# Kernel optimization log

Measured on AMD Instinct MI355X. Metric: run time of the kernel, lower is better.

The kernel has to match this reference:

```python
import jax, jax.numpy as jnp
import numpy as np
import math

EPS = 1e-5
ANGLES = [0, 30, 45, 60, 90, 135]
SIGMA = 0.3
POOL = 7  # top-hat neighbourhood


def make_masks(H, W):
    # Soft Gaussian stripe masks, one per angle: [A, H, W]
    ys = np.linspace(-1.0, 1.0, H)
    xs = np.linspace(-1.0, 1.0, W)
    gy, gx = np.meshgrid(ys, xs, indexing='ij')
    ms = []
    for a in ANGLES:
        t = a * math.pi / 180.0
        perp = gx * (-math.sin(t)) + gy * math.cos(t)
        ms.append(np.exp(-0.5 * (perp / SIGMA) ** 2))
    return jnp.asarray(np.stack(ms, axis=0), dtype=jnp.float32)


def dwconv1d(x, w):
    # x: [B, C, L], w: [C, 1, K] depthwise, 'same' padding (odd K)
    return jax.lax.conv_general_dilated(
        x, w, window_strides=(1,), padding='SAME',
        feature_group_count=x.shape[1],
        dimension_numbers=('NCH', 'OIH', 'NCH'))


def bn(x, gamma, beta, axes, pshape):
    # Training-mode batch norm (biased variance, as in torch forward)
    mean = x.mean(axes, keepdims=True)
    var = x.var(axes, keepdims=True)
    return (x - mean) * jax.lax.rsqrt(var + EPS) * gamma.reshape(pshape) + beta.reshape(pshape)


def maxpool_same(x, k):
    # torch MaxPool2d(k, stride=1, padding=k//2): pad with -inf
    p = k // 2
    return jax.lax.reduce_window(
        x, -jnp.inf, jax.lax.max,
        window_dimensions=(1, 1, k, k), window_strides=(1, 1, 1, 1),
        padding=[(0, 0), (0, 0), (p, p), (p, p)])


def setup_inputs() -> dict:
    key = jax.random.key(0)
    ks = jax.random.split(key, 8)
    B, C, H, W = 128, 576, 28, 28
    K = 3
    x = jax.random.normal(ks[0], (B, C, H, W), dtype=jnp.float32)
    h_w = jax.random.normal(ks[1], (C, 1, K), dtype=jnp.float32) * 0.2
    v_w = jax.random.normal(ks[2], (C, 1, K), dtype=jnp.float32) * 0.2
    f_w = jax.random.normal(ks[3], (C,), dtype=jnp.float32) * 0.2  # 1x1 dw conv = per-channel scale
    h_g = jnp.ones((C,), jnp.float32); h_b = jnp.zeros((C,), jnp.float32)
    v_g = jnp.ones((C,), jnp.float32); v_b = jnp.zeros((C,), jnp.float32)
    f_g = jnp.ones((C,), jnp.float32); f_b = jnp.zeros((C,), jnp.float32)
    return {"x": x, "h_w": h_w, "h_g": h_g, "h_b": h_b,
            "v_w": v_w, "v_g": v_g, "v_b": v_b,
            "f_w": f_w, "f_g": f_g, "f_b": f_b}


def reference(x, h_w, h_g, h_b, v_w, v_g, v_b, f_w, f_g, f_b):
    B, C, H, W = x.shape
    # Horizontal stream: mean over W -> dw conv1d over H -> BN1d -> sigmoid -> [B,C,H,1]
    ph = x.mean(axis=-1)                                   # [B, C, H]
    A_h = jax.nn.sigmoid(bn(dwconv1d(ph, h_w), h_g, h_b, (0, 2), (1, C, 1)))[..., None]
    # Vertical stream: mean over H -> dw conv1d over W -> BN1d -> sigmoid -> [B,C,1,W]
    pv = x.mean(axis=-2)                                   # [B, C, W]
    A_v = jax.nn.sigmoid(bn(dwconv1d(pv, v_w), v_g, v_b, (0, 2), (1, C, 1)))[:, :, None, :]
    # Focal spot stream: white top-hat -> per-channel scale -> BN2d -> sigmoid
    spots = maxpool_same(x, POOL) - x                      # [B, C, H, W]
    A_f = jax.nn.sigmoid(bn(spots * f_w[None, :, None, None], f_g, f_b, (0, 2, 3), (1, C, 1, 1)))
    # Orientation bank: masked global means, sigmoid per angle, mean over angles
    masks = make_masks(H, W)                               # [A, H, W]
    resp = jnp.einsum('bchw,ahw->bca', x, masks) / (H * W) # [B, C, A]
    A_t = jax.nn.sigmoid(resp).mean(axis=-1)[:, :, None, None]
    return x * A_h * A_v * A_f * A_t
```

## Files before the change

### kernel.cpp

```cpp
#include <hip/hip_runtime.h>
#include <math.h>

#define B 128
#define C 576
#define H 28
#define W 28
#define HW 784
#define NPLANE (B * C)
#define RMROWS 34
#define LOG2E 1.4426950408889634f

typedef float nfloat4 __attribute__((ext_vector_type(4)));
typedef _Float16 half2v __attribute__((ext_vector_type(2)));

__device__ __forceinline__ float sigm2(float z2) { return 1.f / (1.f + exp2f(-z2)); }

__device__ __forceinline__ float4 fmax4(float4 a, float4 b) {
    a.x = fmaxf(a.x, b.x); a.y = fmaxf(a.y, b.y);
    a.z = fmaxf(a.z, b.z); a.w = fmaxf(a.w, b.w);
    return a;
}

__device__ __forceinline__ float4 hmax13(float4 Mv, float4 Lv, float4 Rv) {
    float mm   = fmaxf(fmaxf(Mv.x, Mv.y), fmaxf(Mv.z, Mv.w));
    float l23  = fmaxf(Lv.z, Lv.w);
    float l123 = fmaxf(Lv.y, l23);
    float r01  = fmaxf(Rv.x, Rv.y);
    float r012 = fmaxf(r01, Rv.z);
    float4 o;
    o.x = fmaxf(l123, mm);
    o.y = fmaxf(l23, fmaxf(mm, Rv.x));
    o.z = fmaxf(Lv.w, fmaxf(mm, r01));
    o.w = fmaxf(mm, r012);
    return o;
}

__device__ __forceinline__ float dpp_sum64(float v) {
    int t;
    t = __builtin_amdgcn_update_dpp(0, __float_as_int(v), 0x111, 0xf, 0xf, true);  v += __int_as_float(t);
    t = __builtin_amdgcn_update_dpp(0, __float_as_int(v), 0x112, 0xf, 0xf, true);  v += __int_as_float(t);
    t = __builtin_amdgcn_update_dpp(0, __float_as_int(v), 0x114, 0xf, 0xf, true);  v += __int_as_float(t);
    t = __builtin_amdgcn_update_dpp(0, __float_as_int(v), 0x118, 0xf, 0xf, true);  v += __int_as_float(t);
    t = __builtin_amdgcn_update_dpp(0, __float_as_int(v), 0x142, 0xa, 0xf, false); v += __int_as_float(t);
    t = __builtin_amdgcn_update_dpp(0, __float_as_int(v), 0x143, 0xc, 0xf, false); v += __int_as_float(t);
    return v;
}

__device__ __forceinline__ float dpp_sum32(float v) {
    int t;
    t = __builtin_amdgcn_update_dpp(0, __float_as_int(v), 0x111, 0xf, 0xf, true);  v += __int_as_float(t);
    t = __builtin_amdgcn_update_dpp(0, __float_as_int(v), 0x112, 0xf, 0xf, true);  v += __int_as_float(t);
    t = __builtin_amdgcn_update_dpp(0, __float_as_int(v), 0x114, 0xf, 0xf, true);  v += __int_as_float(t);
    t = __builtin_amdgcn_update_dpp(0, __float_as_int(v), 0x118, 0xf, 0xf, true);  v += __int_as_float(t);
    t = __builtin_amdgcn_update_dpp(0, __float_as_int(v), 0x142, 0xa, 0xf, false); v += __int_as_float(t);
    return v;
}

__device__ __forceinline__ float rlane(float v, int n) {
    return __int_as_float(__builtin_amdgcn_readlane(__float_as_int(v), n));
}

__device__ __forceinline__ void wave_lds_fence() {
    asm volatile("s_waitcnt lgkmcnt(0)" ::: "memory");
    __builtin_amdgcn_sched_barrier(0);
}

__device__ __forceinline__ float dot4h(half2v vlo, half2v vhi, uint2 md, float acc) {
    half2v mlo = __builtin_bit_cast(half2v, md.x);
    half2v mhi = __builtin_bit_cast(half2v, md.y);
#if __has_builtin(__builtin_amdgcn_fdot2)
    acc = __builtin_amdgcn_fdot2(vlo, mlo, acc, false);
    acc = __builtin_amdgcn_fdot2(vhi, mhi, acc, false);
#else
    acc += (float)vlo.x * (float)mlo.x + (float)vlo.y * (float)mlo.y
         + (float)vhi.x * (float)mhi.x + (float)vhi.y * (float)mhi.y;
#endif
    return acc;
}

__global__ void k0_init(_Float16* __restrict__ masksf16, float* __restrict__ acc) {
    int idx = blockIdx.x * 256 + threadIdx.x;
    if (idx < 6 * C) acc[idx] = 0.f;
    if (idx < 4 * HW) {
        int a = idx / HW;
        int p = idx - a * HW;
        int r = p / W;
        int col = p - r * W;
        const float degs[4] = {30.f, 45.f, 60.f, 135.f};
        float t = degs[a] * 0.017453292519943295f;
        float gy = -1.f + r * (2.f / 27.f);
        float gx = -1.f + col * (2.f / 27.f);
        float perp = gx * (-sinf(t)) + gy * cosf(t);
        float z = perp * (1.f / 0.3f);
        masksf16[idx] = (_Float16)expf(-0.5f * z * z);
    }
}

__global__ __launch_bounds__(256, 7) void k1_stats(
    const float* __restrict__ x,
    const float* __restrict__ h_w, const float* __restrict__ v_w,
    const float* __restrict__ f_w, const _Float16* __restrict__ masksf16,
    float* __restrict__ yh, float* __restrict__ yv,
    float* __restrict__ at, float* __restrict__ acc)
{
    const int tid = threadIdx.x;
    const int wvi = __builtin_amdgcn_readfirstlane(tid >> 6);
    const int l   = tid & 63;
    const int plane = blockIdx.x * 4 + wvi;
    const int c = plane % C;
    const float* xp = x + (size_t)plane * HW;

    __shared__ __align__(16) float uA[4][RMROWS * W];
    __shared__ __align__(16) float cpA[4][196];
    __shared__ __align__(16) float rpA[4][196];
    float* rm  = uA[wvi];
    float* sxv = rm + 3 * W;
    float* cp  = cpA[wvi];
    float* rp  = rpA[wvi];

    const int r0 = l / 7;
    const int u  = l - r0 * 7;
    const int q  = u * 4;
    const int qL = u ? q - 4 : 0;
    const int qR = (u < 6) ? q + 4 : 24;
    const bool act = (l < 49);

    const uint2* mk2p = (const uint2*)masksf16;

    float4 Mv[4];
    float fs = 0.f, fss = 0.f;
    float o30 = 0.f, o45 = 0.f, o60 = 0.f, o135 = 0.f;

    if (act) {
        float4 ca = make_float4(0.f, 0.f, 0.f, 0.f);
        float rw[4];
        #pragma unroll
        for (int k = 0; k < 4; ++k) {
            const int unit = l + 49 * k;
            float4 v = ((const float4*)xp)[unit];
            Mv[k] = v;
            ((float4*)sxv)[unit] = v;
            ca.x += v.x; ca.y += v.y; ca.z += v.z; ca.w += v.w;
            rw[k] = (v.x + v.y) + (v.z + v.w);
            half2v vlo = __builtin_bit_cast(half2v, __builtin_amdgcn_cvt_pkrtz(v.x, v.y));
            half2v vhi = __builtin_bit_cast(half2v, __builtin_amdgcn_cvt_pkrtz(v.z, v.w));
            o30  = dot4h(vlo, vhi, mk2p[unit],           o30);
            o45  = dot4h(vlo, vhi, mk2p[196 + unit],     o45);
            o60  = dot4h(vlo, vhi, mk2p[2 * 196 + unit], o60);
            o135 = dot4h(vlo, vhi, mk2p[3 * 196 + unit], o135);
        }
        ((float4*)cp)[l] = ca;
        ((float4*)rp)[l] = make_float4(rw[0], rw[1], rw[2], rw[3]);
    }
    wave_lds_fence();

    if (act) {
        #pragma unroll
        for (int k = 0; k < 4; ++k) {
            const int r = r0 + 7 * k;
            const float* row = sxv + r * W;
            float4 Lv = *(const float4*)(row + qL);
            float4 Rv = *(const float4*)(row + qR);
            float4 hv = hmax13(Mv[k], Lv, Rv);
            *(float4*)(rm + (r + 3) * W + q) = hv;
            if (k == 0 && r0 == 0) {
                *(float4*)(rm + 0 * W + q) = hv;
                *(float4*)(rm + 1 * W + q) = hv;
                *(float4*)(rm + 2 * W + q) = hv;
            }
            if (k == 3 && r0 == 6) {
                *(float4*)(rm + 31 * W + q) = hv;
                *(float4*)(rm + 32 * W + q) = hv;
                *(float4*)(rm + 33 * W + q) = hv;
            }
        }
    }
    wave_lds_fence();

    if (act) {
        #pragma unroll
        for (int k = 0; k < 4; ++k) {
            const int r = r0 + 7 * k;
            const float* vb = rm + r * W + q;
            float4 m = *(const float4*)vb;
            m = fmax4(m, *(const float4*)(vb + W));
            m = fmax4(m, *(const float4*)(vb + 2 * W));
            m = fmax4(m, *(const float4*)(vb + 3 * W));
            m = fmax4(m, *(const float4*)(vb + 4 * W));
            m = fmax4(m, *(const float4*)(vb + 5 * W));
            m = fmax4(m, *(const float4*)(vb + 6 * W));
            float s0 = m.x - Mv[k].x;
            float s1 = m.y - Mv[k].y;
            float s2 = m.z - Mv[k].z;
            float s3 = m.w - Mv[k].w;
            fs  += (s0 + s1) + (s2 + s3);
            fss += (s0 * s0 + s1 * s1) + (s2 * s2 + s3 * s3);
        }
    }

    const int idx = l & 31;
    const bool inr = (idx < 28);
    float ssum = 0.f;
    if (inr) {
        const float* bp;
        int st;
        if (l < 32) { bp = rp + (l % 7) * 28 + (l / 7); st = 4; }
        else        { bp = cp + idx;                    st = 28; }
        ssum = ((bp[0] + bp[st]) + (bp[2 * st] + bp[3 * st]))
             + ((bp[4 * st] + bp[5 * st]) + bp[6 * st]);
    }
    float pmean = ssum * (1.f / 28.f);

    float g = -1.f + (float)idx * (2.f / 27.f);
    float mg = exp2f(-8.014972687f * g * g);
    float packC = inr ? ssum * mg : 0.f;

    const float w0 = (l < 32) ? h_w[c * 3]     : v_w[c * 3];
    const float w1 = (l < 32) ? h_w[c * 3 + 1] : v_w[c * 3 + 1];
    const float w2 = (l < 32) ? h_w[c * 3 + 2] : v_w[c * 3 + 2];
    float y = 0.f;
    {
        float pm = __shfl_up(pmean, 1);
        float pp = __shfl_down(pmean, 1);
        if (inr) {
            float a = (idx > 0) ? pm : 0.f;
            float d = (idx < 27) ? pp : 0.f;
            y = w0 * a + w1 * pmean + w2 * d;
            if (l < 32) yh[(size_t)plane * H + idx] = y;
            else        yv[(size_t)plane * W + idx] = y;
        }
    }
    float packA = y;
    float packB = y * y;

    fs   = dpp_sum64(fs);   fss  = dpp_sum64(fss);
    o30  = dpp_sum64(o30);  o45  = dpp_sum64(o45);
    o60  = dpp_sum64(o60);  o135 = dpp_sum64(o135);
    packA = dpp_sum32(packA);
    packB = dpp_sum32(packB);
    packC = dpp_sum32(packC);
    float yhs  = rlane(packA, 31), yvs  = rlane(packA, 63);
    float yhq  = rlane(packB, 31), yvq  = rlane(packB, 63);
    float r0s  = rlane(packC, 31), r90s = rlane(packC, 63);

    if (l == 63) {
        const float s784 = LOG2E / (float)HW;
        float t = sigm2(r0s * s784) + sigm2(o30 * s784) + sigm2(o45 * s784)
                + sigm2(o60 * s784) + sigm2(r90s * s784) + sigm2(o135 * s784);
        at[plane] = t * (1.f / 6.f);
        const float fwc = f_w[c];
        atomicAdd(&acc[0 * C + c], yhs);
        atomicAdd(&acc[1 * C + c], yhq);
        atomicAdd(&acc[2 * C + c], yvs);
        atomicAdd(&acc[3 * C + c], yvq);
        atomicAdd(&acc[4 * C + c], fs * fwc);
        atomicAdd(&acc[5 * C + c], fss * fwc * fwc);
    }
}

__global__ __launch_bounds__(64) void k2_params(
    const float* __restrict__ acc, const float* __restrict__ f_w,
    const float* __restrict__ hg, const float* __restrict__ hb,
    const float* __restrict__ vg, const float* __restrict__ vb,
    const float* __restrict__ fg, const float* __restrict__ fb,
    float* __restrict__ params)
{
    int c = blockIdx.x * 64 + threadIdx.x;
    if (c >= C) return;
    const float inv_nh = 1.f / (float)(B * H);
    const float inv_nf = 1.f / (float)(B * HW);
    float m, v, sc;
    m = acc[c] * inv_nh;
    v = acc[C + c] * inv_nh - m * m;
    sc = hg[c] * rsqrtf(v + 1e-5f);
    params[c * 8 + 0] = sc * LOG2E; params[c * 8 + 1] = (hb[c] - m * sc) * LOG2E;

    m = acc[2 * C + c] * inv_nh;
    v = acc[3 * C + c] * inv_nh - m * m;
    sc = vg[c] * rsqrtf(v + 1e-5f);
    params[c * 8 + 2] = sc * LOG2E; params[c * 8 + 3] = (vb[c] - m * sc) * LOG2E;

    m = acc[4 * C + c] * inv_nf;
    v = acc[5 * C + c] * inv_nf - m * m;
    sc = fg[c] * rsqrtf(v + 1e-5f);
    params[c * 8 + 4] = sc * f_w[c] * LOG2E;
    params[c * 8 + 5] = (fb[c] - m * sc) * LOG2E;
}

__global__ __launch_bounds__(256, 8) void k3_apply(
    const float* __restrict__ x,
    const float* __restrict__ yh, const float* __restrict__ yv,
    const float* __restrict__ at, const float* __restrict__ params,
    float* __restrict__ out)
{
    const int tid = threadIdx.x;
    const int wvi = __builtin_amdgcn_readfirstlane(tid >> 6);
    const int l   = tid & 63;
    const int plane = blockIdx.x * 4 + wvi;
    const int c = plane % C;
    const float* xp = x + (size_t)plane * HW;

    __shared__ __align__(16) float uA[4][RMROWS * W];
    float* rm  = uA[wvi];
    float* sxv = rm + 3 * W;

    const int r0 = l / 7;
    const int u  = l - r0 * 7;
    const int q  = u * 4;
    const int qL = u ? q - 4 : 0;
    const int qR = (u < 6) ? q + 4 : 24;
    const bool act = (l < 49);

    const float4 pA = *(const float4*)(params + c * 8);
    const float2 pB = *(const float2*)(params + c * 8 + 4);
    const float atv = at[plane];

    float4 Mv[4];

    if (act) {
        #pragma unroll
        for (int k = 0; k < 4; ++k) {
            const int unit = l + 49 * k;
            Mv[k] = ((const float4*)xp)[unit];
            ((float4*)sxv)[unit] = Mv[k];
        }
    }
    wave_lds_fence();

    if (act) {
        #pragma unroll
        for (int k = 0; k < 4; ++k) {
            const int r = r0 + 7 * k;
            const float* row = sxv + r * W;
            float4 Lv = *(const float4*)(row + qL);
            float4 Rv = *(const float4*)(row + qR);
            float4 hv = hmax13(Mv[k], Lv, Rv);
            *(float4*)(rm + (r + 3) * W + q) = hv;
            if (k == 0 && r0 == 0) {
                *(float4*)(rm + 0 * W + q) = hv;
                *(float4*)(rm + 1 * W + q) = hv;
                *(float4*)(rm + 2 * W + q) = hv;
            }
            if (k == 3 && r0 == 6) {
                *(float4*)(rm + 31 * W + q) = hv;
                *(float4*)(rm + 32 * W + q) = hv;
                *(float4*)(rm + 33 * W + q) = hv;
            }
        }
    }
    wave_lds_fence();

    if (act) {
        float4 yv4;
        yv4.x = yv[(size_t)plane * W + q];
        yv4.y = yv[(size_t)plane * W + q + 1];
        yv4.z = yv[(size_t)plane * W + q + 2];
        yv4.w = yv[(size_t)plane * W + q + 3];
        float4 av;
        av.x = sigm2(pA.z * yv4.x + pA.w);
        av.y = sigm2(pA.z * yv4.y + pA.w);
        av.z = sigm2(pA.z * yv4.z + pA.w);
        av.w = sigm2(pA.z * yv4.w + pA.w);
        nfloat4* op = (nfloat4*)(out + (size_t)plane * HW);
        #pragma unroll
        for (int k = 0; k < 4; ++k) {
            const int r = r0 + 7 * k;
            const float* vb = rm + r * W + q;
            float4 m = *(const float4*)vb;
            m = fmax4(m, *(const float4*)(vb + W));
            m = fmax4(m, *(const float4*)(vb + 2 * W));
            m = fmax4(m, *(const float4*)(vb + 3 * W));
            m = fmax4(m, *(const float4*)(vb + 4 * W));
            m = fmax4(m, *(const float4*)(vb + 5 * W));
            m = fmax4(m, *(const float4*)(vb + 6 * W));
            float ahk = sigm2(pA.x * yh[(size_t)plane * H + r] + pA.y) * atv;
            nfloat4 o;
            o.x = Mv[k].x * ahk * av.x * sigm2(fmaf(pB.x, m.x, fmaf(-pB.x, Mv[k].x, pB.y)));
            o.y = Mv[k].y * ahk * av.y * sigm2(fmaf(pB.x, m.y, fmaf(-pB.x, Mv[k].y, pB.y)));
            o.z = Mv[k].z * ahk * av.z * sigm2(fmaf(pB.x, m.z, fmaf(-pB.x, Mv[k].z, pB.y)));
            o.w = Mv[k].w * ahk * av.w * sigm2(fmaf(pB.x, m.w, fmaf(-pB.x, Mv[k].w, pB.y)));
            __builtin_nontemporal_store(o, &op[l + 49 * k]);
        }
    }
}

extern "C" void kernel_launch(void* const* d_in, const int* in_sizes, int n_in,
                              void* d_out, int out_size, void* d_ws, size_t ws_size,
                              hipStream_t stream) {
    const float* x   = (const float*)d_in[0];
    const float* h_w = (const float*)d_in[1];
    const float* h_g = (const float*)d_in[2];
    const float* h_b = (const float*)d_in[3];
    const float* v_w = (const float*)d_in[4];
    const float* v_g = (const float*)d_in[5];
    const float* v_b = (const float*)d_in[6];
    const float* f_w = (const float*)d_in[7];
    const float* f_g = (const float*)d_in[8];
    const float* f_b = (const float*)d_in[9];
    float* out = (float*)d_out;
    float* ws = (float*)d_ws;

    _Float16* masksf16 = (_Float16*)ws;
    float* acc    = ws + 1568;
    float* params = ws + 5024;
    float* at     = ws + 9632;
    float* yh     = ws + 83360;
    float* yv     = ws + 2147744;

    k0_init<<<14, 256, 0, stream>>>(masksf16, acc);
    k1_stats<<<NPLANE / 4, 256, 0, stream>>>(x, h_w, v_w, f_w, masksf16, yh, yv, at, acc);
    k2_params<<<9, 64, 0, stream>>>(acc, f_w, h_g, h_b, v_g, v_b, f_g, f_b, params);
    k3_apply<<<NPLANE / 4, 256, 0, stream>>>(x, yh, yv, at, params, out);
}
```

Baseline: 172.5 us.

## Give each lane 4 consecutive rows in stats kernel to share vertical max window

The stats kernel now maps each lane to four consecutive rows (rows 4*r0..4*r0+3) instead of rows strided by 7. The vertical 7-row max can then share a common 4-row middle across the four outputs, so each lane reads 10 LDS rows instead of 28 and does fewer max ops. The row/column sum gathers are re-indexed to match the new layout. The six full-wave DPP reductions are replaced by cross-half xor shuffles that pack pairs of values into 32-lane halves, followed by 32-lane DPP sums and readlane. This changes the global load coalescing pattern (strided row chunks per lane), which may affect memory efficiency.

```diff
diff --git a/kernel.cpp b/kernel.cpp
--- a/kernel.cpp
+++ b/kernel.cpp
@@ -33,17 +33,6 @@
     o.z = fmaxf(Lv.w, fmaxf(mm, r01));
     o.w = fmaxf(mm, r012);
     return o;
-}
-
-__device__ __forceinline__ float dpp_sum64(float v) {
-    int t;
-    t = __builtin_amdgcn_update_dpp(0, __float_as_int(v), 0x111, 0xf, 0xf, true);  v += __int_as_float(t);
-    t = __builtin_amdgcn_update_dpp(0, __float_as_int(v), 0x112, 0xf, 0xf, true);  v += __int_as_float(t);
-    t = __builtin_amdgcn_update_dpp(0, __float_as_int(v), 0x114, 0xf, 0xf, true);  v += __int_as_float(t);
-    t = __builtin_amdgcn_update_dpp(0, __float_as_int(v), 0x118, 0xf, 0xf, true);  v += __int_as_float(t);
-    t = __builtin_amdgcn_update_dpp(0, __float_as_int(v), 0x142, 0xa, 0xf, false); v += __int_as_float(t);
-    t = __builtin_amdgcn_update_dpp(0, __float_as_int(v), 0x143, 0xc, 0xf, false); v += __int_as_float(t);
-    return v;
 }
 
 __device__ __forceinline__ float dpp_sum32(float v) {
@@ -124,6 +113,7 @@
     const int qL = u ? q - 4 : 0;
     const int qR = (u < 6) ? q + 4 : 24;
     const bool act = (l < 49);
+    const int rbase = 4 * r0;
 
     const uint2* mk2p = (const uint2*)masksf16;
 
@@ -135,13 +125,13 @@
         float4 ca = make_float4(0.f, 0.f, 0.f, 0.f);
         float rw[4];
         #pragma unroll
-        for (int k = 0; k < 4; ++k) {
-            const int unit = l + 49 * k;
+        for (int j = 0; j < 4; ++j) {
+            const int unit = (rbase + j) * 7 + u;
             float4 v = ((const float4*)xp)[unit];
-            Mv[k] = v;
+            Mv[j] = v;
             ((float4*)sxv)[unit] = v;
             ca.x += v.x; ca.y += v.y; ca.z += v.z; ca.w += v.w;
-            rw[k] = (v.x + v.y) + (v.z + v.w);
+            rw[j] = (v.x + v.y) + (v.z + v.w);
             half2v vlo = __builtin_bit_cast(half2v, __builtin_amdgcn_cvt_pkrtz(v.x, v.y));
             half2v vhi = __builtin_bit_cast(half2v, __builtin_amdgcn_cvt_pkrtz(v.z, v.w));
             o30  = dot4h(vlo, vhi, mk2p[unit],           o30);
@@ -151,6 +141,204 @@
         }
         ((float4*)cp)[l] = ca;
         ((float4*)rp)[l] = make_float4(rw[0], rw[1], rw[2], rw[3]);
+    }
+    wave_lds_fence();
+
+    if (act) {
+        #pragma unroll
+        for (int j = 0; j < 4; ++j) {
+            const int r = rbase + j;
+            const float* row = sxv + r * W;
+            float4 Lv = *(const float4*)(row + qL);
+            float4 Rv = *(const float4*)(row + qR);
+            float4 hv = hmax13(Mv[j], Lv, Rv);
+            *(float4*)(rm + (r + 3) * W + q) = hv;
+            if (j == 0 && r0 == 0) {
+                *(float4*)(rm + 0 * W + q) = hv;
+                *(float4*)(rm + 1 * W + q) = hv;
+                *(float4*)(rm + 2 * W + q) = hv;
+            }
+            if (j == 3 && r0 == 6) {
+                *(float4*)(rm + 31 * W + q) = hv;
+                *(float4*)(rm + 32 * W + q) = hv;
+                *(float4*)(rm + 33 * W + q) = hv;
+            }
+        }
+    }
+    wave_lds_fence();
+
+    if (act) {
+        const float* vb = rm + rbase * W + q;
+        float4 v0 = *(const float4*)(vb);
+        float4 v1 = *(const float4*)(vb + W);
+        float4 v2 = *(const float4*)(vb + 2 * W);
+        float4 v3 = *(const float4*)(vb + 3 * W);
+        float4 v4 = *(const float4*)(vb + 4 * W);
+        float4 v5 = *(const float4*)(vb + 5 * W);
+        float4 v6 = *(const float4*)(vb + 6 * W);
+        float4 v7 = *(const float4*)(vb + 7 * W);
+        float4 v8 = *(const float4*)(vb + 8 * W);
+        float4 v9 = *(const float4*)(vb + 9 * W);
+        float4 cc = fmax4(fmax4(v3, v4), fmax4(v5, v6));
+        float4 m0 = fmax4(fmax4(v0, v1), fmax4(v2, cc));
+        float4 m1 = fmax4(fmax4(v1, v2), fmax4(cc, v7));
+        float4 m2 = fmax4(fmax4(v2, cc), fmax4(v7, v8));
+        float4 m3 = fmax4(fmax4(cc, v7), fmax4(v8, v9));
+        float4 mm[4] = {m0, m1, m2, m3};
+        #pragma unroll
+        for (int j = 0; j < 4; ++j) {
+            float s0 = mm[j].x - Mv[j].x;
+            float s1 = mm[j].y - Mv[j].y;
+            float s2 = mm[j].z - Mv[j].z;
+            float s3 = mm[j].w - Mv[j].w;
+            fs  += (s0 + s1) + (s2 + s3);
+            fss += (s0 * s0 + s1 * s1) + (s2 * s2 + s3 * s3);
+        }
+    }
+
+    const int idx = l & 31;
+    const bool inr = (idx < 28);
+    float ssum = 0.f;
+    if (inr) {
+        if (l < 32) {
+            const float* bp = rp + (idx >> 2) * 28 + (idx & 3);
+            ssum = ((bp[0] + bp[4]) + (bp[8] + bp[12]))
+                 + ((bp[16] + bp[20]) + bp[24]);
+        } else {
+            const float* bp = cp + idx;
+            ssum = ((bp[0] + bp[28]) + (bp[56] + bp[84]))
+                 + ((bp[112] + bp[140]) + bp[168]);
+        }
+    }
+    float pmean = ssum * (1.f / 28.f);
+
+    float g = -1.f + (float)idx * (2.f / 27.f);
+    float mg = exp2f(-8.014972687f * g * g);
+    float packC = inr ? ssum * mg : 0.f;
+
+    const float w0 = (l < 32) ? h_w[c * 3]     : v_w[c * 3];
+    const float w1 = (l < 32) ? h_w[c * 3 + 1] : v_w[c * 3 + 1];
+    const float w2 = (l < 32) ? h_w[c * 3 + 2] : v_w[c * 3 + 2];
+    float y = 0.f;
+    {
+        float pm = __shfl_up(pmean, 1);
+        float pp = __shfl_down(pmean, 1);
+        if (inr) {
+            float a = (idx > 0) ? pm : 0.f;
+            float d = (idx < 27) ? pp : 0.f;
+            y = w0 * a + w1 * pmean + w2 * d;
+            if (l < 32) yh[(size_t)plane * H + idx] = y;
+            else        yv[(size_t)plane * W + idx] = y;
+        }
+    }
+    float packA = y;
+    float packB = y * y;
+
+    float fsx  = fs  + __shfl_xor(fs,  32, 64);
+    float fssx = fss + __shfl_xor(fss, 32, 64);
+    float pF = (l < 32) ? fsx : fssx;
+    float oAx = o30 + __shfl_xor(o30, 32, 64);
+    float oBx = o45 + __shfl_xor(o45, 32, 64);
+    float pO1 = (l < 32) ? oAx : oBx;
+    float oCx = o60  + __shfl_xor(o60,  32, 64);
+    float oDx = o135 + __shfl_xor(o135, 32, 64);
+    float pO2 = (l < 32) ? oCx : oDx;
+
+    pF    = dpp_sum32(pF);
+    pO1   = dpp_sum32(pO1);
+    pO2   = dpp_sum32(pO2);
+    packA = dpp_sum32(packA);
+    packB = dpp_sum32(packB);
+    packC = dpp_sum32(packC);
+
+    float fsT   = rlane(pF, 31),    fssT = rlane(pF, 63);
+    float o30T  = rlane(pO1, 31),   o45T = rlane(pO1, 63);
+    float o60T  = rlane(pO2, 31),  o135T = rlane(pO2, 63);
+    float yhs   = rlane(packA, 31),  yvs = rlane(packA, 63);
+    float yhq   = rlane(packB, 31),  yvq = rlane(packB, 63);
+    float r0s   = rlane(packC, 31), r90s = rlane(packC, 63);
+
+    if (l == 63) {
+        const float s784 = LOG2E / (float)HW;
+        float t = sigm2(r0s * s784) + sigm2(o30T * s784) + sigm2(o45T * s784)
+                + sigm2(o60T * s784) + sigm2(r90s * s784) + sigm2(o135T * s784);
+        at[plane] = t * (1.f / 6.f);
+        const float fwc = f_w[c];
+        atomicAdd(&acc[0 * C + c], yhs);
+        atomicAdd(&acc[1 * C + c], yhq);
+        atomicAdd(&acc[2 * C + c], yvs);
+        atomicAdd(&acc[3 * C + c], yvq);
+        atomicAdd(&acc[4 * C + c], fsT * fwc);
+        atomicAdd(&acc[5 * C + c], fssT * fwc * fwc);
+    }
+}
+
+__global__ __launch_bounds__(64) void k2_params(
+    const float* __restrict__ acc, const float* __restrict__ f_w,
+    const float* __restrict__ hg, const float* __restrict__ hb,
+    const float* __restrict__ vg, const float* __restrict__ vb,
+    const float* __restrict__ fg, const float* __restrict__ fb,
+    float* __restrict__ params)
+{
+    int c = blockIdx.x * 64 + threadIdx.x;
+    if (c >= C) return;
+    const float inv_nh = 1.f / (float)(B * H);
+    const float inv_nf = 1.f / (float)(B * HW);
+    float m, v, sc;
+    m = acc[c] * inv_nh;
+    v = acc[C + c] * inv_nh - m * m;
+    sc = hg[c] * rsqrtf(v + 1e-5f);
+    params[c * 8 + 0] = sc * LOG2E; params[c * 8 + 1] = (hb[c] - m * sc) * LOG2E;
+
+    m = acc[2 * C + c] * inv_nh;
+    v = acc[3 * C + c] * inv_nh - m * m;
+    sc = vg[c] * rsqrtf(v + 1e-5f);
+    params[c * 8 + 2] = sc * LOG2E; params[c * 8 + 3] = (vb[c] - m * sc) * LOG2E;
+
+    m = acc[4 * C + c] * inv_nf;
+    v = acc[5 * C + c] * inv_nf - m * m;
+    sc = fg[c] * rsqrtf(v + 1e-5f);
+    params[c * 8 + 4] = sc * f_w[c] * LOG2E;
+    params[c * 8 + 5] = (fb[c] - m * sc) * LOG2E;
+}
+
+__global__ __launch_bounds__(256, 8) void k3_apply(
+    const float* __restrict__ x,
+    const float* __restrict__ yh, const float* __restrict__ yv,
+    const float* __restrict__ at, const float* __restrict__ params,
+    float* __restrict__ out)
+{
+    const int tid = threadIdx.x;
+    const int wvi = __builtin_amdgcn_readfirstlane(tid >> 6);
+    const int l   = tid & 63;
+    const int plane = blockIdx.x * 4 + wvi;
+    const int c = plane % C;
+    const float* xp = x + (size_t)plane * HW;
+
+    __shared__ __align__(16) float uA[4][RMROWS * W];
+    float* rm  = uA[wvi];
+    float* sxv = rm + 3 * W;
+
+    const int r0 = l / 7;
+    const int u  = l - r0 * 7;
+    const int q  = u * 4;
+    const int qL = u ? q - 4 : 0;
+    const int qR = (u < 6) ? q + 4 : 24;
+    const bool act = (l < 49);
+
+    const float4 pA = *(const float4*)(params + c * 8);
+    const float2 pB = *(const float2*)(params + c * 8 + 4);
+    const float atv = at[plane];
+
+    float4 Mv[4];
+
+    if (act) {
+        #pragma unroll
+        for (int k = 0; k < 4; ++k) {
+            const int unit = l + 49 * k;
+            Mv[k] = ((const float4*)xp)[unit];
+            ((float4*)sxv)[unit] = Mv[k];
+        }
     }
     wave_lds_fence();
 
@@ -178,179 +366,6 @@
     wave_lds_fence();
 
     if (act) {
-        #pragma unroll
-        for (int k = 0; k < 4; ++k) {
-            const int r = r0 + 7 * k;
-            const float* vb = rm + r * W + q;
-            float4 m = *(const float4*)vb;
-            m = fmax4(m, *(const float4*)(vb + W));
-            m = fmax4(m, *(const float4*)(vb + 2 * W));
-            m = fmax4(m, *(const float4*)(vb + 3 * W));
-            m = fmax4(m, *(const float4*)(vb + 4 * W));
-            m = fmax4(m, *(const float4*)(vb + 5 * W));
-            m = fmax4(m, *(const float4*)(vb + 6 * W));
-            float s0 = m.x - Mv[k].x;
-            float s1 = m.y - Mv[k].y;
-            float s2 = m.z - Mv[k].z;
-            float s3 = m.w - Mv[k].w;
-            fs  += (s0 + s1) + (s2 + s3);
-            fss += (s0 * s0 + s1 * s1) + (s2 * s2 + s3 * s3);
-        }
-    }
-
-    const int idx = l & 31;
-    const bool inr = (idx < 28);
-    float ssum = 0.f;
-    if (inr) {
-        const float* bp;
-        int st;
-        if (l < 32) { bp = rp + (l % 7) * 28 + (l / 7); st = 4; }
-        else        { bp = cp + idx;                    st = 28; }
-        ssum = ((bp[0] + bp[st]) + (bp[2 * st] + bp[3 * st]))
-             + ((bp[4 * st] + bp[5 * st]) + bp[6 * st]);
-    }
-    float pmean = ssum * (1.f / 28.f);
-
-    float g = -1.f + (float)idx * (2.f / 27.f);
-    float mg = exp2f(-8.014972687f * g * g);
-    float packC = inr ? ssum * mg : 0.f;
-
-    const float w0 = (l < 32) ? h_w[c * 3]     : v_w[c * 3];
-    const float w1 = (l < 32) ? h_w[c * 3 + 1] : v_w[c * 3 + 1];
-    const float w2 = (l < 32) ? h_w[c * 3 + 2] : v_w[c * 3 + 2];
-    float y = 0.f;
-    {
-        float pm = __shfl_up(pmean, 1);
-        float pp = __shfl_down(pmean, 1);
-        if (inr) {
-            float a = (idx > 0) ? pm : 0.f;
-            float d = (idx < 27) ? pp : 0.f;
-            y = w0 * a + w1 * pmean + w2 * d;
-            if (l < 32) yh[(size_t)plane * H + idx] = y;
-            else        yv[(size_t)plane * W + idx] = y;
-        }
-    }
-    float packA = y;
-    float packB = y * y;
-
-    fs   = dpp_sum64(fs);   fss  = dpp_sum64(fss);
-    o30  = dpp_sum64(o30);  o45  = dpp_sum64(o45);
-    o60  = dpp_sum64(o60);  o135 = dpp_sum64(o135);
-    packA = dpp_sum32(packA);
-    packB = dpp_sum32(packB);
-    packC = dpp_sum32(packC);
-    float yhs  = rlane(packA, 31), yvs  = rlane(packA, 63);
-    float yhq  = rlane(packB, 31), yvq  = rlane(packB, 63);
-    float r0s  = rlane(packC, 31), r90s = rlane(packC, 63);
-
-    if (l == 63) {
-        const float s784 = LOG2E / (float)HW;
-        float t = sigm2(r0s * s784) + sigm2(o30 * s784) + sigm2(o45 * s784)
-                + sigm2(o60 * s784) + sigm2(r90s * s784) + sigm2(o135 * s784);
-        at[plane] = t * (1.f / 6.f);
-        const float fwc = f_w[c];
-        atomicAdd(&acc[0 * C + c], yhs);
-        atomicAdd(&acc[1 * C + c], yhq);
-        atomicAdd(&acc[2 * C + c], yvs);
-        atomicAdd(&acc[3 * C + c], yvq);
-        atomicAdd(&acc[4 * C + c], fs * fwc);
-        atomicAdd(&acc[5 * C + c], fss * fwc * fwc);
-    }
-}
-
-__global__ __launch_bounds__(64) void k2_params(
-    const float* __restrict__ acc, const float* __restrict__ f_w,
-    const float* __restrict__ hg, const float* __restrict__ hb,
-    const float* __restrict__ vg, const float* __restrict__ vb,
-    const float* __restrict__ fg, const float* __restrict__ fb,
-    float* __restrict__ params)
-{
-    int c = blockIdx.x * 64 + threadIdx.x;
-    if (c >= C) return;
-    const float inv_nh = 1.f / (float)(B * H);
-    const float inv_nf = 1.f / (float)(B * HW);
-    float m, v, sc;
-    m = acc[c] * inv_nh;
-    v = acc[C + c] * inv_nh - m * m;
-    sc = hg[c] * rsqrtf(v + 1e-5f);
-    params[c * 8 + 0] = sc * LOG2E; params[c * 8 + 1] = (hb[c] - m * sc) * LOG2E;
-
-    m = acc[2 * C + c] * inv_nh;
-    v = acc[3 * C + c] * inv_nh - m * m;
-    sc = vg[c] * rsqrtf(v + 1e-5f);
-    params[c * 8 + 2] = sc * LOG2E; params[c * 8 + 3] = (vb[c] - m * sc) * LOG2E;
-
-    m = acc[4 * C + c] * inv_nf;
-    v = acc[5 * C + c] * inv_nf - m * m;
-    sc = fg[c] * rsqrtf(v + 1e-5f);
-    params[c * 8 + 4] = sc * f_w[c] * LOG2E;
-    params[c * 8 + 5] = (fb[c] - m * sc) * LOG2E;
-}
-
-__global__ __launch_bounds__(256, 8) void k3_apply(
-    const float* __restrict__ x,
-    const float* __restrict__ yh, const float* __restrict__ yv,
-    const float* __restrict__ at, const float* __restrict__ params,
-    float* __restrict__ out)
-{
-    const int tid = threadIdx.x;
-    const int wvi = __builtin_amdgcn_readfirstlane(tid >> 6);
-    const int l   = tid & 63;
-    const int plane = blockIdx.x * 4 + wvi;
-    const int c = plane % C;
-    const float* xp = x + (size_t)plane * HW;
-
-    __shared__ __align__(16) float uA[4][RMROWS * W];
-    float* rm  = uA[wvi];
-    float* sxv = rm + 3 * W;
-
-    const int r0 = l / 7;
-    const int u  = l - r0 * 7;
-    const int q  = u * 4;
-    const int qL = u ? q - 4 : 0;
-    const int qR = (u < 6) ? q + 4 : 24;
-    const bool act = (l < 49);
-
-    const float4 pA = *(const float4*)(params + c * 8);
-    const float2 pB = *(const float2*)(params + c * 8 + 4);
-    const float atv = at[plane];
-
-    float4 Mv[4];
-
-    if (act) {
-        #pragma unroll
-        for (int k = 0; k < 4; ++k) {
-            const int unit = l + 49 * k;
-            Mv[k] = ((const float4*)xp)[unit];
-            ((float4*)sxv)[unit] = Mv[k];
-        }
-    }
-    wave_lds_fence();
-
-    if (act) {
-        #pragma unroll
-        for (int k = 0; k < 4; ++k) {
-            const int r = r0 + 7 * k;
-            const float* row = sxv + r * W;
-            float4 Lv = *(const float4*)(row + qL);
-            float4 Rv = *(const float4*)(row + qR);
-            float4 hv = hmax13(Mv[k], Lv, Rv);
-            *(float4*)(rm + (r + 3) * W + q) = hv;
-            if (k == 0 && r0 == 0) {
-                *(float4*)(rm + 0 * W + q) = hv;
-                *(float4*)(rm + 1 * W + q) = hv;
-                *(float4*)(rm + 2 * W + q) = hv;
-            }
-            if (k == 3 && r0 == 6) {
-                *(float4*)(rm + 31 * W + q) = hv;
-                *(float4*)(rm + 32 * W + q) = hv;
-                *(float4*)(rm + 33 * W + q) = hv;
-            }
-        }
-    }
-    wave_lds_fence();
-
-    if (act) {
         float4 yv4;
         yv4.x = yv[(size_t)plane * W + q];
         yv4.y = yv[(size_t)plane * W + q + 1];
```

Result: no change. 169.5 us (-1.8%).
